# Kernel tuning notes

Measured on AMD Instinct MI355X. Metric: run time of the kernel, lower is better.

Reference implementation:

```python
import jax, jax.numpy as jnp
import numpy as np

GAMMA = 1.0        # softmin temperature
BANDWIDTH = 0      # 0 => no Sakoe-Chiba band (numba code only skips when 0 < bw < |i-j|)
BIG = 1e30         # finite stand-in for +inf: exp(-BIG/gamma) underflows to exactly 0 in fp32,
                   # reproducing the inf-initialized R/SigR softmin ratios without NaNs
B, N, M = 32, 512, 512


def setup_inputs() -> dict:
    k1, k2 = jax.random.split(jax.random.key(0))
    D = jax.random.uniform(k1, (B, N, M), dtype=jnp.float32)    # pairwise distances (>= 0)
    Sig = jax.random.uniform(k2, (B, N, M), dtype=jnp.float32)  # per-cell uncertainty
    return {"D": D, "Sig": Sig}


def _soft_dtw(D, Sig):
    """uDTW forward DP (compute_softdtw), vectorized over anti-diagonal wavefronts.
    Returns jnp.stack([R[:, N, M], SigR[:, N, M]]) of shape (2, B)."""
    b, n, m = D.shape
    alpha = 1.0 / GAMMA
    # Dp[i, j] == D_new[i, j] = D[i-1, j-1] with zero border (indices 0..N, 0..M)
    Dp = jnp.pad(D, ((0, 0), (1, 0), (1, 0)))
    Sp = jnp.pad(Sig, ((0, 0), (1, 0), (1, 0)))
    iarr = jnp.arange(n + 1)

    def diag(A, d):
        # A[:, i, d - i] for i = 0..N, zero where j out of [0, M]
        j = d - iarr
        vals = A[:, iarr, jnp.clip(j, 0, m)]
        return jnp.where((j >= 0) & (j <= m), vals, 0.0)

    def shift(x, fill):
        # x[:, i-1] (index i-1 along the diagonal buffer)
        return jnp.concatenate([jnp.full((b, 1), fill, x.dtype), x[:, :-1]], axis=1)

    # diagonal buffers indexed by i; diag d=0 holds R[0,0]=0, rest inf(BIG); diag d=1 all inf
    r2 = jnp.full((b, n + 1), BIG, jnp.float32).at[:, 0].set(0.0)
    r1 = jnp.full((b, n + 1), BIG, jnp.float32)
    s2 = jnp.full((b, n + 1), BIG, jnp.float32).at[:, 0].set(0.0)
    s1 = jnp.full((b, n + 1), BIG, jnp.float32)

    def step(carry, d):
        r2, r1, s2, s1 = carry  # R/SigR diagonals d-2 and d-1
        j = d - iarr
        valid = (iarr >= 1) & (j >= 1) & (j <= m)
        if BANDWIDTH > 0:
            valid = valid & (jnp.abs(iarr - j) <= BANDWIDTH)
        # softmin ratios from R neighbors: (i-1,j-1)=prev2 shifted, (i-1,j)=prev1 shifted, (i,j-1)=prev1
        rr0 = -alpha * shift(r2, BIG)
        rr1 = -alpha * shift(r1, BIG)
        rr2 = -alpha * r1
        rmax = jnp.maximum(jnp.maximum(rr0, rr1), rr2)
        e0 = jnp.exp(rr0 - rmax)
        e1 = jnp.exp(rr1 - rmax)
        e2 = jnp.exp(rr2 - rmax)
        inv = 1.0 / (e0 + e1 + e2)
        p0, p1, p2 = e0 * inv, e1 * inv, e2 * inv
        dDd, dD1, dD2 = diag(Dp, d), diag(Dp, d - 1), diag(Dp, d - 2)
        dSd, dS1, dS2 = diag(Sp, d), diag(Sp, d - 1), diag(Sp, d - 2)
        # R[i,j] = D[i-1,j-1] + softmin-weighted avg of D_new neighbors (uDTW recurrence)
        newR = jnp.where(valid, dDd + p0 * shift(dD2, 0.0) + p1 * shift(dD1, 0.0) + p2 * dD1, BIG)
        newS = jnp.where(valid, dSd + p0 * shift(dS2, 0.0) + p1 * shift(dS1, 0.0) + p2 * dS1, BIG)
        return (r1, newR, s1, newS), None

    (_, rlast, _, slast), _ = jax.lax.scan(step, (r2, r1, s2, s1), jnp.arange(2, n + m + 1))
    # last anti-diagonal d = N + M contains cell (N, M) at index i = N
    return jnp.stack([rlast[:, n], slast[:, n]])  # (2, B)


def reference(D, Sig):
    return _soft_dtw(D, Sig)
```

## Files before the change

### kernel.cpp

```cpp
#include <hip/hip_runtime.h>


constexpr int N = 512;
constexpr int M = 512;
constexpr int BATCH = 32;
constexpr int NM = N + M;
constexpr int K = 16;
constexpr int NB = 64;
constexpr int PHASES = NB + 7;
constexpr float NL2E = -1.4426950408889634f;
constexpr float NLN2 = -0.6931471805599453f;

__device__ __forceinline__ float lane_shr1(float x) {
  return __int_as_float(
      __builtin_amdgcn_update_dpp(0, __float_as_int(x), 0x138, 0xf, 0xf, true));
}

__global__ __launch_bounds__(512, 2)
void softdtw_fwd(const float* __restrict__ D,
                 const float* __restrict__ Sig,
                 float* __restrict__ out) {
  const int b = blockIdx.x;
  const int t = threadIdx.x;
  const int w = t >> 6;
  const int lane = t & 63;
  const bool l0 = (lane == 0);
  const float4* Drow4 = (const float4*)(D + ((size_t)b * N + t) * M);

  __shared__ float2 edge[8][640];
  for (int idx = t; idx < 8 * 640; idx += 512)
    ((float2*)edge)[idx] = make_float2(0.f, 0.f);

  float eSelf = 0.f, dSelfL = 0.f;
  float eN2 = (t == 0) ? 1.f : 0.f, dN2L = 0.f;

  float sgA = 0.f, sg0 = 0.f, sg1 = 0.f, sg2 = 0.f;
  if (t == N - 1) {
    const float* Sb = Sig + (size_t)b * N * M;
    sgA = Sb[(size_t)(N - 1) * M + (M - 1)];
    sg0 = Sb[(size_t)(N - 2) * M + (M - 2)];
    sg1 = Sb[(size_t)(N - 2) * M + (M - 1)];
    sg2 = Sb[(size_t)(N - 1) * M + (M - 2)];
  }
  __syncthreads();

  const int Bl = 4 * w;
  const int Bh = 4 * w + 35;

  for (int p = 0; p < PHASES; ++p) {
    const int B = p - w;
    if (B >= Bl && B <= Bh) {
      const int d0 = 2 + B * K;
      const int c0 = d0 - t - 2;

      const int q0 = c0 >> 2;
      int qa = min(max(q0 + 0, 0), 127);
      int qb = min(max(q0 + 1, 0), 127);
      int qc = min(max(q0 + 2, 0), 127);
      int qd = min(max(q0 + 3, 0), 127);
      int qe = min(max(q0 + 4, 0), 127);
      float4 r0 = Drow4[qa], r1 = Drow4[qb], r2q = Drow4[qc],
             r3 = Drow4[qd], r4 = Drow4[qe];

      const int s = c0 & 3;
      const bool s2 = (s & 2) != 0, s1b = (s & 1) != 0;
      float x0  = s2 ? r0.z  : r0.x,  x1  = s2 ? r0.w  : r0.y,
            x2  = s2 ? r1.x  : r0.z,  x3  = s2 ? r1.y  : r0.w,
            x4  = s2 ? r1.z  : r1.x,  x5  = s2 ? r1.w  : r1.y,
            x6  = s2 ? r2q.x : r1.z,  x7  = s2 ? r2q.y : r1.w,
            x8  = s2 ? r2q.z : r2q.x, x9  = s2 ? r2q.w : r2q.y,
            x10 = s2 ? r3.x  : r2q.z, x11 = s2 ? r3.y  : r2q.w,
            x12 = s2 ? r3.z  : r3.x,  x13 = s2 ? r3.w  : r3.y,
            x14 = s2 ? r4.x  : r3.z,  x15 = s2 ? r4.y  : r3.w,
            x16 = s2 ? r4.z  : r4.x,  x17 = s2 ? r4.w  : r4.y;
      float g0  = s1b ? x1  : x0,  g1  = s1b ? x2  : x1,
            g2  = s1b ? x3  : x2,  g3  = s1b ? x4  : x3,
            g4  = s1b ? x5  : x4,  g5  = s1b ? x6  : x5,
            g6  = s1b ? x7  : x6,  g7  = s1b ? x8  : x7,
            g8  = s1b ? x9  : x8,  g9  = s1b ? x10 : x9,
            g10 = s1b ? x11 : x10, g11 = s1b ? x12 : x11,
            g12 = s1b ? x13 : x12, g13 = s1b ? x14 : x13,
            g14 = s1b ? x15 : x14, g15 = s1b ? x16 : x15;

      float4 n0, n1, n2, n3, n4, n5, n6, n7;
      if (w > 0) {
        const int cp0 = d0 - 64 * w - 2;
        const float4* ep = (const float4*)&edge[w - 1][64 + cp0];
        n0 = ep[0]; n1 = ep[1]; n2 = ep[2]; n3 = ep[3];
        n4 = ep[4]; n5 = ep[5]; n6 = ep[6]; n7 = ep[7];
      } else {
        n0 = n1 = n2 = n3 = n4 = n5 = n6 = n7 = make_float4(0.f, 0.f, 0.f, 0.f);
      }

      float2* eput = &edge[w][64 + c0];

#define STEP(kk, GK, NE, ND)                                                   \
      {                                                                        \
        const int d = d0 + (kk);                                               \
        const int c = c0 + (kk);                                               \
        const bool valid = ((unsigned)c) < 512u;                               \
        float ddL = (GK) * NL2E;                                               \
        ddL = valid ? ddL : 0.f;                                               \
        float sE = lane_shr1(eSelf);                                           \
        float sD = lane_shr1(dSelfL);                                          \
        sE = l0 ? (NE) : sE;                                                   \
        sD = l0 ? (ND) : sD;                                                   \
        const float e0 = eN2, e1 = sE, e2 = eSelf;                             \
        const float sum = (e0 + e2) + e1;                                      \
        const float inv = __builtin_amdgcn_rcpf(sum);                          \
        const float numL = fmaf(e0, dN2L, fmaf(e1, sD, e2 * dSelfL));          \
        const float rr = fmaf(inv, numL, ddL);                                 \
        float newE = __builtin_amdgcn_exp2f(rr);                               \
        newE = valid ? newE : 0.f;                                             \
        if (d == NM && t == N - 1) {                                           \
          out[b] = rr * NLN2;                                                  \
          out[BATCH + b] = sgA + inv * (e0 * sg0 + e1 * sg1 + e2 * sg2);       \
        }                                                                      \
        eN2 = e1; dN2L = sD;                                                   \
        eSelf = newE; dSelfL = ddL;                                            \
        eput[kk] = make_float2(newE, ddL);                                     \
      }

      STEP(0,  g0,  n0.x, n0.y)  STEP(1,  g1,  n0.z, n0.w)
      STEP(2,  g2,  n1.x, n1.y)  STEP(3,  g3,  n1.z, n1.w)
      STEP(4,  g4,  n2.x, n2.y)  STEP(5,  g5,  n2.z, n2.w)
      STEP(6,  g6,  n3.x, n3.y)  STEP(7,  g7,  n3.z, n3.w)
      STEP(8,  g8,  n4.x, n4.y)  STEP(9,  g9,  n4.z, n4.w)
      STEP(10, g10, n5.x, n5.y)  STEP(11, g11, n5.z, n5.w)
      STEP(12, g12, n6.x, n6.y)  STEP(13, g13, n6.z, n6.w)
      STEP(14, g14, n7.x, n7.y)  STEP(15, g15, n7.z, n7.w)
#undef STEP
    }
    __syncthreads();
  }
}

extern "C" void kernel_launch(void* const* d_in, const int* in_sizes, int n_in,
                              void* d_out, int out_size, void* d_ws, size_t ws_size,
                              hipStream_t stream) {
  const float* D   = (const float*)d_in[0];
  const float* Sig = (const float*)d_in[1];
  float* out = (float*)d_out;
  softdtw_fwd<<<dim3(BATCH), dim3(512), 0, stream>>>(D, Sig, out);
}
```

Baseline: 197.7 us.

## Double chunk length per phase and prefetch next phase's D row into registers

Each wavefront phase now covers 32 anti-diagonals instead of 16, which halves the number of phases and block-wide barriers. The D values for the next phase are loaded into registers during the current phase so that global-load latency overlaps with the serial DP steps. The cost is higher register pressure (about 36 extra floats of prefetch plus 64 edge floats) and a longer pipeline fill and drain, since warps start two phases apart. It also risks spills under the 512x2 launch bounds.

```diff
diff --git a/kernel.cpp b/kernel.cpp
--- a/kernel.cpp
+++ b/kernel.cpp
@@ -5,8 +5,8 @@
 constexpr int M = 512;
 constexpr int BATCH = 32;
 constexpr int NM = N + M;
-constexpr int K = 16;
-constexpr int NB = 64;
+constexpr int K = 32;
+constexpr int NB = 32;
 constexpr int PHASES = NB + 7;
 constexpr float NL2E = -1.4426950408889634f;
 constexpr float NLN2 = -0.6931471805599453f;
@@ -16,6 +16,10 @@
       __builtin_amdgcn_update_dpp(0, __float_as_int(x), 0x138, 0xf, 0xf, true));
 }
 
+__device__ __forceinline__ int qclamp(int q) {
+  return q < 0 ? 0 : (q > 127 ? 127 : q);
+}
+
 __global__ __launch_bounds__(512, 2)
 void softdtw_fwd(const float* __restrict__ D,
                  const float* __restrict__ Sig,
@@ -23,8 +27,7 @@
   const int b = blockIdx.x;
   const int t = threadIdx.x;
   const int w = t >> 6;
-  const int lane = t & 63;
-  const bool l0 = (lane == 0);
+  const bool l0 = ((t & 63) == 0);
   const float4* Drow4 = (const float4*)(D + ((size_t)b * N + t) * M);
 
   __shared__ float2 edge[8][640];
@@ -42,55 +45,88 @@
     sg1 = Sb[(size_t)(N - 2) * M + (M - 1)];
     sg2 = Sb[(size_t)(N - 1) * M + (M - 2)];
   }
+
+  const int Bl = 2 * w, Bh = 2 * w + 17;
+
+  float4 r0, r1, r2, r3, r4, r5, r6, r7, r8;
+  {
+    const int q = (32 * Bl - t) >> 2;
+    r0 = Drow4[qclamp(q + 0)]; r1 = Drow4[qclamp(q + 1)];
+    r2 = Drow4[qclamp(q + 2)]; r3 = Drow4[qclamp(q + 3)];
+    r4 = Drow4[qclamp(q + 4)]; r5 = Drow4[qclamp(q + 5)];
+    r6 = Drow4[qclamp(q + 6)]; r7 = Drow4[qclamp(q + 7)];
+    r8 = Drow4[qclamp(q + 8)];
+  }
   __syncthreads();
-
-  const int Bl = 4 * w;
-  const int Bh = 4 * w + 35;
 
   for (int p = 0; p < PHASES; ++p) {
     const int B = p - w;
+    const int nB = B + 1;
+    const bool dopre = (nB >= Bl) && (nB <= Bh);
+
+    float4 p0, p1, p2, p3, p4, p5, p6, p7, p8;
+    if (dopre) {
+      const int q = (32 * nB - t) >> 2;
+      p0 = Drow4[qclamp(q + 0)]; p1 = Drow4[qclamp(q + 1)];
+      p2 = Drow4[qclamp(q + 2)]; p3 = Drow4[qclamp(q + 3)];
+      p4 = Drow4[qclamp(q + 4)]; p5 = Drow4[qclamp(q + 5)];
+      p6 = Drow4[qclamp(q + 6)]; p7 = Drow4[qclamp(q + 7)];
+      p8 = Drow4[qclamp(q + 8)];
+    }
+
     if (B >= Bl && B <= Bh) {
       const int d0 = 2 + B * K;
       const int c0 = d0 - t - 2;
 
-      const int q0 = c0 >> 2;
-      int qa = min(max(q0 + 0, 0), 127);
-      int qb = min(max(q0 + 1, 0), 127);
-      int qc = min(max(q0 + 2, 0), 127);
-      int qd = min(max(q0 + 3, 0), 127);
-      int qe = min(max(q0 + 4, 0), 127);
-      float4 r0 = Drow4[qa], r1 = Drow4[qb], r2q = Drow4[qc],
-             r3 = Drow4[qd], r4 = Drow4[qe];
+      float4 n0, n1, n2, n3, n4, n5, n6, n7, n8, n9, n10, n11, n12, n13, n14, n15;
+      if (w > 0) {
+        const float4* ep = (const float4*)&edge[w - 1][64 + (d0 - 64 * w - 2)];
+        n0 = ep[0];  n1 = ep[1];  n2 = ep[2];  n3 = ep[3];
+        n4 = ep[4];  n5 = ep[5];  n6 = ep[6];  n7 = ep[7];
+        n8 = ep[8];  n9 = ep[9];  n10 = ep[10]; n11 = ep[11];
+        n12 = ep[12]; n13 = ep[13]; n14 = ep[14]; n15 = ep[15];
+      } else {
+        const float4 z = make_float4(0.f, 0.f, 0.f, 0.f);
+        n0 = n1 = n2 = n3 = n4 = n5 = n6 = n7 = z;
+        n8 = n9 = n10 = n11 = n12 = n13 = n14 = n15 = z;
+      }
 
       const int s = c0 & 3;
       const bool s2 = (s & 2) != 0, s1b = (s & 1) != 0;
-      float x0  = s2 ? r0.z  : r0.x,  x1  = s2 ? r0.w  : r0.y,
-            x2  = s2 ? r1.x  : r0.z,  x3  = s2 ? r1.y  : r0.w,
-            x4  = s2 ? r1.z  : r1.x,  x5  = s2 ? r1.w  : r1.y,
-            x6  = s2 ? r2q.x : r1.z,  x7  = s2 ? r2q.y : r1.w,
-            x8  = s2 ? r2q.z : r2q.x, x9  = s2 ? r2q.w : r2q.y,
-            x10 = s2 ? r3.x  : r2q.z, x11 = s2 ? r3.y  : r2q.w,
-            x12 = s2 ? r3.z  : r3.x,  x13 = s2 ? r3.w  : r3.y,
-            x14 = s2 ? r4.x  : r3.z,  x15 = s2 ? r4.y  : r3.w,
-            x16 = s2 ? r4.z  : r4.x,  x17 = s2 ? r4.w  : r4.y;
-      float g0  = s1b ? x1  : x0,  g1  = s1b ? x2  : x1,
-            g2  = s1b ? x3  : x2,  g3  = s1b ? x4  : x3,
-            g4  = s1b ? x5  : x4,  g5  = s1b ? x6  : x5,
-            g6  = s1b ? x7  : x6,  g7  = s1b ? x8  : x7,
-            g8  = s1b ? x9  : x8,  g9  = s1b ? x10 : x9,
-            g10 = s1b ? x11 : x10, g11 = s1b ? x12 : x11,
-            g12 = s1b ? x13 : x12, g13 = s1b ? x14 : x13,
-            g14 = s1b ? x15 : x14, g15 = s1b ? x16 : x15;
-
-      float4 n0, n1, n2, n3, n4, n5, n6, n7;
-      if (w > 0) {
-        const int cp0 = d0 - 64 * w - 2;
-        const float4* ep = (const float4*)&edge[w - 1][64 + cp0];
-        n0 = ep[0]; n1 = ep[1]; n2 = ep[2]; n3 = ep[3];
-        n4 = ep[4]; n5 = ep[5]; n6 = ep[6]; n7 = ep[7];
-      } else {
-        n0 = n1 = n2 = n3 = n4 = n5 = n6 = n7 = make_float4(0.f, 0.f, 0.f, 0.f);
-      }
+      const float
+        f0 = r0.x, f1 = r0.y, f2 = r0.z, f3 = r0.w,
+        f4 = r1.x, f5 = r1.y, f6 = r1.z, f7 = r1.w,
+        f8 = r2.x, f9 = r2.y, f10 = r2.z, f11 = r2.w,
+        f12 = r3.x, f13 = r3.y, f14 = r3.z, f15 = r3.w,
+        f16 = r4.x, f17 = r4.y, f18 = r4.z, f19 = r4.w,
+        f20 = r5.x, f21 = r5.y, f22 = r5.z, f23 = r5.w,
+        f24 = r6.x, f25 = r6.y, f26 = r6.z, f27 = r6.w,
+        f28 = r7.x, f29 = r7.y, f30 = r7.z, f31 = r7.w,
+        f32 = r8.x, f33 = r8.y, f34 = r8.z, f35 = r8.w;
+      const float
+        x0  = s2 ? f2  : f0,  x1  = s2 ? f3  : f1,  x2  = s2 ? f4  : f2,
+        x3  = s2 ? f5  : f3,  x4  = s2 ? f6  : f4,  x5  = s2 ? f7  : f5,
+        x6  = s2 ? f8  : f6,  x7  = s2 ? f9  : f7,  x8  = s2 ? f10 : f8,
+        x9  = s2 ? f11 : f9,  x10 = s2 ? f12 : f10, x11 = s2 ? f13 : f11,
+        x12 = s2 ? f14 : f12, x13 = s2 ? f15 : f13, x14 = s2 ? f16 : f14,
+        x15 = s2 ? f17 : f15, x16 = s2 ? f18 : f16, x17 = s2 ? f19 : f17,
+        x18 = s2 ? f20 : f18, x19 = s2 ? f21 : f19, x20 = s2 ? f22 : f20,
+        x21 = s2 ? f23 : f21, x22 = s2 ? f24 : f22, x23 = s2 ? f25 : f23,
+        x24 = s2 ? f26 : f24, x25 = s2 ? f27 : f25, x26 = s2 ? f28 : f26,
+        x27 = s2 ? f29 : f27, x28 = s2 ? f30 : f28, x29 = s2 ? f31 : f29,
+        x30 = s2 ? f32 : f30, x31 = s2 ? f33 : f31, x32 = s2 ? f34 : f32;
+      const float
+        g0  = s1b ? x1  : x0,  g1  = s1b ? x2  : x1,  g2  = s1b ? x3  : x2,
+        g3  = s1b ? x4  : x3,  g4  = s1b ? x5  : x4,  g5  = s1b ? x6  : x5,
+        g6  = s1b ? x7  : x6,  g7  = s1b ? x8  : x7,  g8  = s1b ? x9  : x8,
+        g9  = s1b ? x10 : x9,  g10 = s1b ? x11 : x10, g11 = s1b ? x12 : x11,
+        g12 = s1b ? x13 : x12, g13 = s1b ? x14 : x13, g14 = s1b ? x15 : x14,
+        g15 = s1b ? x16 : x15, g16 = s1b ? x17 : x16, g17 = s1b ? x18 : x17,
+        g18 = s1b ? x19 : x18, g19 = s1b ? x20 : x19, g20 = s1b ? x21 : x20,
+        g21 = s1b ? x22 : x21, g22 = s1b ? x23 : x22, g23 = s1b ? x24 : x23,
+        g24 = s1b ? x25 : x24, g25 = s1b ? x26 : x25, g26 = s1b ? x27 : x26,
+        g27 = s1b ? x28 : x27, g28 = s1b ? x29 : x28, g29 = s1b ? x30 : x29,
+        g30 = s1b ? x31 : x30, g31 = s1b ? x32 : x31;
 
       float2* eput = &edge[w][64 + c0];
 
@@ -120,16 +156,25 @@
         eSelf = newE; dSelfL = ddL;                                            \
         eput[kk] = make_float2(newE, ddL);                                     \
       }
+#define STEP2(m, GA, GB)                                                       \
+      STEP(2 * m, GA, n##m.x, n##m.y)                                          \
+      STEP(2 * m + 1, GB, n##m.z, n##m.w)
 
-      STEP(0,  g0,  n0.x, n0.y)  STEP(1,  g1,  n0.z, n0.w)
-      STEP(2,  g2,  n1.x, n1.y)  STEP(3,  g3,  n1.z, n1.w)
-      STEP(4,  g4,  n2.x, n2.y)  STEP(5,  g5,  n2.z, n2.w)
-      STEP(6,  g6,  n3.x, n3.y)  STEP(7,  g7,  n3.z, n3.w)
-      STEP(8,  g8,  n4.x, n4.y)  STEP(9,  g9,  n4.z, n4.w)
-      STEP(10, g10, n5.x, n5.y)  STEP(11, g11, n5.z, n5.w)
-      STEP(12, g12, n6.x, n6.y)  STEP(13, g13, n6.z, n6.w)
-      STEP(14, g14, n7.x, n7.y)  STEP(15, g15, n7.z, n7.w)
+      STEP2(0,  g0,  g1)   STEP2(1,  g2,  g3)
+      STEP2(2,  g4,  g5)   STEP2(3,  g6,  g7)
+      STEP2(4,  g8,  g9)   STEP2(5,  g10, g11)
+      STEP2(6,  g12, g13)  STEP2(7,  g14, g15)
+      STEP2(8,  g16, g17)  STEP2(9,  g18, g19)
+      STEP2(10, g20, g21)  STEP2(11, g22, g23)
+      STEP2(12, g24, g25)  STEP2(13, g26, g27)
+      STEP2(14, g28, g29)  STEP2(15, g30, g31)
+#undef STEP2
 #undef STEP
+    }
+
+    if (dopre) {
+      r0 = p0; r1 = p1; r2 = p2; r3 = p3; r4 = p4;
+      r5 = p5; r6 = p6; r7 = p7; r8 = p8;
     }
     __syncthreads();
   }
```

Result: slower. 203.7 us (+3.0%).
